# Kernel optimization log

Measured on AMD Instinct MI355X. Metric: run time of the kernel, lower is better.

## Reference

```python
import jax, jax.numpy as jnp
import numpy as np

COST_CLASS = 1.0
COST_BBOX = 5.0
COST_GIOU = 2.0
EPS = 1e-6

BS, Q, T = 8, 900, 256   # batch, num_queries, max_text_len
M = 2000                 # total target boxes concatenated over batch


def setup_inputs() -> dict:
    key = jax.random.key(0)
    k1, k2, k3, k4 = jax.random.split(key, 4)
    pred_logits = jax.random.normal(k1, (BS, Q, T), dtype=jnp.float32)
    pred_boxes = jax.random.uniform(k2, (BS, Q, 4), dtype=jnp.float32, minval=0.05, maxval=0.95)
    tgt_boxes = jax.random.uniform(k3, (M, 4), dtype=jnp.float32, minval=0.05, maxval=0.95)
    tgt_labels = jax.random.uniform(k4, (M, T), dtype=jnp.float32)  # positive token map (soft)
    return {"pred_logits": pred_logits, "pred_boxes": pred_boxes,
            "tgt_boxes": tgt_boxes, "tgt_labels": tgt_labels}


def box_cxcywh_to_xyxy(b):
    cx, cy, w, h = b[..., 0], b[..., 1], b[..., 2], b[..., 3]
    return jnp.stack([cx - 0.5 * w, cy - 0.5 * h, cx + 0.5 * w, cy + 0.5 * h], axis=-1)


def generalized_box_iou(boxes1, boxes2):
    # boxes1: [N,4] xyxy, boxes2: [M,4] xyxy -> [N,M] GIoU
    area1 = (boxes1[:, 2] - boxes1[:, 0]) * (boxes1[:, 3] - boxes1[:, 1])
    area2 = (boxes2[:, 2] - boxes2[:, 0]) * (boxes2[:, 3] - boxes2[:, 1])
    lt = jnp.maximum(boxes1[:, None, :2], boxes2[None, :, :2])  # [N,M,2]
    rb = jnp.minimum(boxes1[:, None, 2:], boxes2[None, :, 2:])
    wh = jnp.clip(rb - lt, 0.0)
    inter = wh[..., 0] * wh[..., 1]
    union = area1[:, None] + area2[None, :] - inter
    iou = inter / (union + EPS)
    lt_e = jnp.minimum(boxes1[:, None, :2], boxes2[None, :, :2])
    rb_e = jnp.maximum(boxes1[:, None, 2:], boxes2[None, :, 2:])
    wh_e = jnp.clip(rb_e - lt_e, 0.0)
    area_e = wh_e[..., 0] * wh_e[..., 1]
    return iou - (area_e - union) / (area_e + EPS)


def reference(pred_logits, pred_boxes, tgt_boxes, tgt_labels):
    bs, q, t = pred_logits.shape
    out_prob = jnp.clip(jax.nn.sigmoid(pred_logits.reshape(bs * q, t)), EPS, 1.0 - EPS)
    pred_bbox = pred_boxes.reshape(bs * q, 4)
    # normalized positive token map
    norm_labels = tgt_labels / (jnp.sum(tgt_labels, axis=1, keepdims=True) + EPS)
    # classification cost: -sum_t p[n,t] * map[m,t]  -> [N, M]
    cost_class = -jnp.einsum('nt,mt->nm', out_prob, norm_labels)
    # L1 box cost (cdist p=1) on cxcywh
    cost_bbox = jnp.sum(jnp.abs(pred_bbox[:, None, :] - tgt_boxes[None, :, :]), axis=-1)
    # GIoU cost on xyxy, clamped to >= -1
    giou = generalized_box_iou(box_cxcywh_to_xyxy(pred_bbox), box_cxcywh_to_xyxy(tgt_boxes))
    cost_giou = -jnp.clip(giou, -1.0)
    C = COST_BBOX * cost_bbox + COST_CLASS * cost_class + COST_GIOU * cost_giou
    return C.reshape(bs, q, -1)
```

## Files before the change

kernel.cpp:

```cpp
#include <hip/hip_runtime.h>
#include <math.h>

#define EPSF 1e-6f

typedef __attribute__((ext_vector_type(8))) short bf16x8;
typedef __attribute__((ext_vector_type(4))) float f32x4;
typedef __attribute__((ext_vector_type(4))) unsigned short u16x4;
typedef __attribute__((ext_vector_type(8))) unsigned short u16x8;

constexpr int TT = 256, MT = 2000, NP = 7200;

static __device__ __forceinline__ unsigned short f2bf(float f) {
    unsigned int u = __float_as_uint(f);
    u += 0x7FFFu + ((u >> 16) & 1u);
    return (unsigned short)(u >> 16);
}
static __device__ __forceinline__ float frcp(float x) { return __builtin_amdgcn_rcpf(x); }

static __device__ __forceinline__ void gload_lds16(const unsigned short* g, unsigned short* l) {
    __builtin_amdgcn_global_load_lds(
        (const __attribute__((address_space(1))) unsigned int*)(g),
        (__attribute__((address_space(3))) unsigned int*)(l),
        16, 0, 0);
}

__global__ __launch_bounds__(256) void prep_kernel(const float* __restrict__ logits,
                                                   const float* __restrict__ lab,
                                                   unsigned short* __restrict__ probs,
                                                   unsigned short* __restrict__ nlab) {
    int b = blockIdx.x;
    if (b < 900) {
        int i = (b * 256 + threadIdx.x) * 8;
        float4 x0 = *reinterpret_cast<const float4*>(logits + i);
        float4 x1 = *reinterpret_cast<const float4*>(logits + i + 4);
        float v[8] = {x0.x, x0.y, x0.z, x0.w, x1.x, x1.y, x1.z, x1.w};
        u16x8 o;
#pragma unroll
        for (int j = 0; j < 8; ++j) {
            float s = frcp(1.0f + __expf(-v[j]));
            s = fminf(fmaxf(s, EPSF), 1.0f - EPSF);
            o[j] = f2bf(s);
        }
        *reinterpret_cast<u16x8*>(probs + i) = o;
    } else {
        int wave = threadIdx.x >> 6;
        int lane = threadIdx.x & 63;
        int m = (b - 900) * 4 + wave;
        float4 v = reinterpret_cast<const float4*>(lab)[m * (TT / 4) + lane];
        float s = v.x + v.y + v.z + v.w;
#pragma unroll
        for (int off = 32; off > 0; off >>= 1) s += __shfl_down(s, off);
        float inv = frcp(__shfl(s, 0) + EPSF);
        u16x4 o;
        o[0] = f2bf(v.x * inv); o[1] = f2bf(v.y * inv);
        o[2] = f2bf(v.z * inv); o[3] = f2bf(v.w * inv);
        *reinterpret_cast<u16x4*>(nlab + m * TT + lane * 4) = o;
    }
}

constexpr int NTX = 113, NTY = 32;

__global__ __launch_bounds__(256) void cost_mfma_kernel(
    const unsigned short* __restrict__ A,
    const unsigned short* __restrict__ B,
    const float* __restrict__ pbox,
    const float* __restrict__ tbox,
    float* __restrict__ out)
{
    __shared__ __align__(16) unsigned short As[64 * 256];
    __shared__ __align__(16) unsigned short Bs[64 * 256];

    int n = blockIdx.x;
    int l = (n & 7) * 452 + (n >> 3);
    const int n0 = (l >> 5) * 64;
    const int m0 = (l & 31) * 64;

    const int tid = threadIdx.x;
    const int lane = tid & 63, wave = tid >> 6;
    const int wr = wave & 1, wc = wave >> 1;
    const int fr = lane & 15, quad = lane >> 4;

    float4 tb[2]; int mj[2]; bool mv[2];
#pragma unroll
    for (int tj = 0; tj < 2; ++tj) {
        int gm = m0 + wc * 32 + tj * 16 + fr;
        mv[tj] = gm < MT; mj[tj] = gm;
        int g = mv[tj] ? gm : MT - 1;
        tb[tj] = *reinterpret_cast<const float4*>(&tbox[g * 4]);
    }
    float4 pbv[2][4]; int pr[2][4];
#pragma unroll
    for (int ti = 0; ti < 2; ++ti)
#pragma unroll
        for (int r = 0; r < 4; ++r) {
            int p = n0 + wr * 32 + ti * 16 + quad * 4 + r;
            pr[ti][r] = p;
            int g = p < NP ? p : NP - 1;
            pbv[ti][r] = *reinterpret_cast<const float4*>(&pbox[g * 4]);
        }

    {
        const int lro = lane >> 5;
        const int lch = lane & 31;
#pragma unroll
        for (int i = 0; i < 8; ++i) {
            int row = wave * 16 + i * 2 + lro;
            int cs = (lch * 16) ^ ((row & 7) << 4);
            int gn = n0 + row; gn = gn > NP - 1 ? NP - 1 : gn;
            int gm = m0 + row; gm = gm > MT - 1 ? MT - 1 : gm;
            gload_lds16(A + gn * TT + (cs >> 1), &As[wave * 4096 + i * 512]);
            gload_lds16(B + gm * TT + (cs >> 1), &Bs[wave * 4096 + i * 512]);
        }
    }
    __syncthreads();

    const char* aB[2]; const char* bB[2];
    const int xs = (fr & 7) << 4;
#pragma unroll
    for (int t = 0; t < 2; ++t) {
        aB[t] = reinterpret_cast<const char*>(As) + (wr * 32 + t * 16 + fr) * 512;
        bB[t] = reinterpret_cast<const char*>(Bs) + (wc * 32 + t * 16 + fr) * 512;
    }

    f32x4 acc[2][2] = {};
#pragma unroll
    for (int kk = 0; kk < 8; ++kk) {
        int cb = (kk * 64 + quad * 16) ^ xs;
        bf16x8 af[2], bg[2];
#pragma unroll
        for (int t = 0; t < 2; ++t) {
            af[t] = *reinterpret_cast<const bf16x8*>(aB[t] + cb);
            bg[t] = *reinterpret_cast<const bf16x8*>(bB[t] + cb);
        }
#pragma unroll
        for (int ti = 0; ti < 2; ++ti)
#pragma unroll
            for (int tj = 0; tj < 2; ++tj)
                acc[ti][tj] = __builtin_amdgcn_mfma_f32_16x16x32_bf16(
                    af[ti], bg[tj], acc[ti][tj], 0, 0, 0);
    }

    float bcx[2], bcy[2], bww[2], bhh[2], bx1[2], by1[2], bx2[2], by2[2], areaB[2];
#pragma unroll
    for (int tj = 0; tj < 2; ++tj) {
        float4 b = tb[tj];
        bcx[tj] = b.x; bcy[tj] = b.y; bww[tj] = b.z; bhh[tj] = b.w;
        bx1[tj] = b.x - 0.5f * b.z; by1[tj] = b.y - 0.5f * b.w;
        bx2[tj] = b.x + 0.5f * b.z; by2[tj] = b.y + 0.5f * b.w;
        areaB[tj] = (bx2[tj] - bx1[tj]) * (by2[tj] - by1[tj]);
    }

#pragma unroll
    for (int ti = 0; ti < 2; ++ti) {
#pragma unroll
        for (int r = 0; r < 4; ++r) {
            int p = pr[ti][r];
            if (p >= NP) continue;
            float4 pb4 = pbv[ti][r];
            float ax1 = pb4.x - 0.5f * pb4.z, ay1 = pb4.y - 0.5f * pb4.w;
            float ax2 = pb4.x + 0.5f * pb4.z, ay2 = pb4.y + 0.5f * pb4.w;
            float areaA = (ax2 - ax1) * (ay2 - ay1);
#pragma unroll
            for (int tj = 0; tj < 2; ++tj) {
                if (!mv[tj]) continue;
                float l1 = fabsf(pb4.x - bcx[tj]) + fabsf(pb4.y - bcy[tj]) +
                           fabsf(pb4.z - bww[tj]) + fabsf(pb4.w - bhh[tj]);
                float ltx = fmaxf(ax1, bx1[tj]), lty = fmaxf(ay1, by1[tj]);
                float rbx = fminf(ax2, bx2[tj]), rby = fminf(ay2, by2[tj]);
                float iw = fmaxf(rbx - ltx, 0.0f), ih = fmaxf(rby - lty, 0.0f);
                float inter = iw * ih;
                float uni = areaA + areaB[tj] - inter;
                float iou = inter * frcp(uni + EPSF);
                float ex1 = fminf(ax1, bx1[tj]), ey1 = fminf(ay1, by1[tj]);
                float ex2 = fmaxf(ax2, bx2[tj]), ey2 = fmaxf(ay2, by2[tj]);
                float ew = fmaxf(ex2 - ex1, 0.0f), eh = fmaxf(ey2 - ey1, 0.0f);
                float areaE = ew * eh;
                float giou = iou - (areaE - uni) * frcp(areaE + EPSF);
                float res = 5.0f * l1 - acc[ti][tj][r] - 2.0f * fmaxf(giou, -1.0f);
                out[p * MT + mj[tj]] = res;
            }
        }
    }
}

extern "C" void kernel_launch(void* const* d_in, const int* in_sizes, int n_in,
                              void* d_out, int out_size, void* d_ws, size_t ws_size,
                              hipStream_t stream) {
    const float* pred_logits = (const float*)d_in[0];
    const float* pred_boxes  = (const float*)d_in[1];
    const float* tgt_boxes   = (const float*)d_in[2];
    const float* tgt_labels  = (const float*)d_in[3];
    float* out = (float*)d_out;

    unsigned short* probs = (unsigned short*)d_ws;
    unsigned short* nlab  = probs + NP * TT;

    prep_kernel<<<900 + 500, 256, 0, stream>>>(pred_logits, tgt_labels, probs, nlab);

    cost_mfma_kernel<<<NTX * NTY, 256, 0, stream>>>(probs, nlab, pred_boxes, tgt_boxes, out);
}
```

Baseline: 111.0 us.

## Load B fragments straight to registers, drop B LDS tile, raise occupancy

Removes the shared-memory staging of the normalized-label (B) tile. Each wave now loads its B MFMA fragments directly from global memory into registers, so LDS use per block is halved. The box loads are moved to after the matmul to lower register pressure, and launch bounds request 4 blocks per SM for higher occupancy. In exchange, B rows are re-read from global/L2 by both row-waves rather than shared through LDS, the direct loads use uncoalesced 16-byte strided accesses, and 16 bf16x8 registers are held per thread.

```diff
diff --git a/kernel.cpp b/kernel.cpp
--- a/kernel.cpp
+++ b/kernel.cpp
@@ -60,7 +60,7 @@
 
 constexpr int NTX = 113, NTY = 32;
 
-__global__ __launch_bounds__(256) void cost_mfma_kernel(
+__global__ __launch_bounds__(256, 4) void cost_mfma_kernel(
     const unsigned short* __restrict__ A,
     const unsigned short* __restrict__ B,
     const float* __restrict__ pbox,
@@ -68,7 +68,6 @@
     float* __restrict__ out)
 {
     __shared__ __align__(16) unsigned short As[64 * 256];
-    __shared__ __align__(16) unsigned short Bs[64 * 256];
 
     int n = blockIdx.x;
     int l = (n & 7) * 452 + (n >> 3);
@@ -80,24 +79,18 @@
     const int wr = wave & 1, wc = wave >> 1;
     const int fr = lane & 15, quad = lane >> 4;
 
-    float4 tb[2]; int mj[2]; bool mv[2];
+    const unsigned short* bp[2];
 #pragma unroll
-    for (int tj = 0; tj < 2; ++tj) {
-        int gm = m0 + wc * 32 + tj * 16 + fr;
-        mv[tj] = gm < MT; mj[tj] = gm;
-        int g = mv[tj] ? gm : MT - 1;
-        tb[tj] = *reinterpret_cast<const float4*>(&tbox[g * 4]);
+    for (int t = 0; t < 2; ++t) {
+        int gb = m0 + wc * 32 + t * 16 + fr; if (gb > MT - 1) gb = MT - 1;
+        bp[t] = B + gb * TT + quad * 8;
     }
-    float4 pbv[2][4]; int pr[2][4];
+    bf16x8 bg[2][8];
 #pragma unroll
-    for (int ti = 0; ti < 2; ++ti)
+    for (int kk = 0; kk < 8; ++kk)
 #pragma unroll
-        for (int r = 0; r < 4; ++r) {
-            int p = n0 + wr * 32 + ti * 16 + quad * 4 + r;
-            pr[ti][r] = p;
-            int g = p < NP ? p : NP - 1;
-            pbv[ti][r] = *reinterpret_cast<const float4*>(&pbox[g * 4]);
-        }
+        for (int t = 0; t < 2; ++t)
+            bg[t][kk] = *reinterpret_cast<const bf16x8*>(bp[t] + kk * 32);
 
     {
         const int lro = lane >> 5;
@@ -107,43 +100,41 @@
             int row = wave * 16 + i * 2 + lro;
             int cs = (lch * 16) ^ ((row & 7) << 4);
             int gn = n0 + row; gn = gn > NP - 1 ? NP - 1 : gn;
-            int gm = m0 + row; gm = gm > MT - 1 ? MT - 1 : gm;
             gload_lds16(A + gn * TT + (cs >> 1), &As[wave * 4096 + i * 512]);
-            gload_lds16(B + gm * TT + (cs >> 1), &Bs[wave * 4096 + i * 512]);
         }
     }
     __syncthreads();
 
-    const char* aB[2]; const char* bB[2];
+    const char* aB[2];
     const int xs = (fr & 7) << 4;
 #pragma unroll
-    for (int t = 0; t < 2; ++t) {
+    for (int t = 0; t < 2; ++t)
         aB[t] = reinterpret_cast<const char*>(As) + (wr * 32 + t * 16 + fr) * 512;
-        bB[t] = reinterpret_cast<const char*>(Bs) + (wc * 32 + t * 16 + fr) * 512;
-    }
 
     f32x4 acc[2][2] = {};
 #pragma unroll
     for (int kk = 0; kk < 8; ++kk) {
         int cb = (kk * 64 + quad * 16) ^ xs;
-        bf16x8 af[2], bg[2];
+        bf16x8 af[2];
 #pragma unroll
-        for (int t = 0; t < 2; ++t) {
+        for (int t = 0; t < 2; ++t)
             af[t] = *reinterpret_cast<const bf16x8*>(aB[t] + cb);
-            bg[t] = *reinterpret_cast<const bf16x8*>(bB[t] + cb);
-        }
 #pragma unroll
         for (int ti = 0; ti < 2; ++ti)
 #pragma unroll
             for (int tj = 0; tj < 2; ++tj)
                 acc[ti][tj] = __builtin_amdgcn_mfma_f32_16x16x32_bf16(
-                    af[ti], bg[tj], acc[ti][tj], 0, 0, 0);
+                    af[ti], bg[tj][kk], acc[ti][tj], 0, 0, 0);
     }
 
     float bcx[2], bcy[2], bww[2], bhh[2], bx1[2], by1[2], bx2[2], by2[2], areaB[2];
+    int mj[2]; bool mv[2];
 #pragma unroll
     for (int tj = 0; tj < 2; ++tj) {
-        float4 b = tb[tj];
+        int gm = m0 + wc * 32 + tj * 16 + fr;
+        mv[tj] = gm < MT; mj[tj] = gm;
+        int g = mv[tj] ? gm : MT - 1;
+        float4 b = *reinterpret_cast<const float4*>(&tbox[g * 4]);
         bcx[tj] = b.x; bcy[tj] = b.y; bww[tj] = b.z; bhh[tj] = b.w;
         bx1[tj] = b.x - 0.5f * b.z; by1[tj] = b.y - 0.5f * b.w;
         bx2[tj] = b.x + 0.5f * b.z; by2[tj] = b.y + 0.5f * b.w;
@@ -154,9 +145,9 @@
     for (int ti = 0; ti < 2; ++ti) {
 #pragma unroll
         for (int r = 0; r < 4; ++r) {
-            int p = pr[ti][r];
+            int p = n0 + wr * 32 + ti * 16 + quad * 4 + r;
             if (p >= NP) continue;
-            float4 pb4 = pbv[ti][r];
+            float4 pb4 = *reinterpret_cast<const float4*>(&pbox[p * 4]);
             float ax1 = pb4.x - 0.5f * pb4.z, ay1 = pb4.y - 0.5f * pb4.w;
             float ax2 = pb4.x + 0.5f * pb4.z, ay2 = pb4.y + 0.5f * pb4.w;
             float areaA = (ax2 - ax1) * (ay2 - ay1);
```

After: 124.4 us. 12.0% more time.

## Make cost kernel persistent and prefetch next tile during epilogue

Applied to the files above, without the earlier changes.

Replaces the one-tile-per-block grid (3616 blocks) with 512 persistent blocks that loop over tiles within an XCD slab, stride 64. After the MFMA phase, the block issues the async global-to-LDS loads and box loads for the next tile before running the GIoU/L1 epilogue and output stores for the current one. This overlaps load latency with the store-heavy epilogue and cuts block launch overhead. In exchange it adds extra syncs per tile and register pressure from the prefetched box data, and it sets launch bounds for two blocks per CU and raises MFMA priority with setprio.

```diff
diff --git a/kernel.cpp b/kernel.cpp
--- a/kernel.cpp
+++ b/kernel.cpp
@@ -59,8 +59,14 @@
 }
 
 constexpr int NTX = 113, NTY = 32;
-
-__global__ __launch_bounds__(256) void cost_mfma_kernel(
+constexpr int SLAB = 452;
+
+struct BoxPre {
+    float4 tb0, tb1;
+    float4 pb[8];
+};
+
+__global__ __launch_bounds__(256, 2) void cost_mfma_kernel(
     const unsigned short* __restrict__ A,
     const unsigned short* __restrict__ B,
     const float* __restrict__ pbox,
@@ -70,116 +76,148 @@
     __shared__ __align__(16) unsigned short As[64 * 256];
     __shared__ __align__(16) unsigned short Bs[64 * 256];
 
-    int n = blockIdx.x;
-    int l = (n & 7) * 452 + (n >> 3);
-    const int n0 = (l >> 5) * 64;
-    const int m0 = (l & 31) * 64;
+    const int x = blockIdx.x & 7;
+    const int kb = blockIdx.x >> 3;
 
     const int tid = threadIdx.x;
     const int lane = tid & 63, wave = tid >> 6;
     const int wr = wave & 1, wc = wave >> 1;
     const int fr = lane & 15, quad = lane >> 4;
 
-    float4 tb[2]; int mj[2]; bool mv[2];
-#pragma unroll
-    for (int tj = 0; tj < 2; ++tj) {
-        int gm = m0 + wc * 32 + tj * 16 + fr;
-        mv[tj] = gm < MT; mj[tj] = gm;
-        int g = mv[tj] ? gm : MT - 1;
-        tb[tj] = *reinterpret_cast<const float4*>(&tbox[g * 4]);
-    }
-    float4 pbv[2][4]; int pr[2][4];
-#pragma unroll
-    for (int ti = 0; ti < 2; ++ti)
-#pragma unroll
-        for (int r = 0; r < 4; ++r) {
-            int p = n0 + wr * 32 + ti * 16 + quad * 4 + r;
-            pr[ti][r] = p;
-            int g = p < NP ? p : NP - 1;
-            pbv[ti][r] = *reinterpret_cast<const float4*>(&pbox[g * 4]);
-        }
-
-    {
-        const int lro = lane >> 5;
-        const int lch = lane & 31;
-#pragma unroll
-        for (int i = 0; i < 8; ++i) {
-            int row = wave * 16 + i * 2 + lro;
-            int cs = (lch * 16) ^ ((row & 7) << 4);
-            int gn = n0 + row; gn = gn > NP - 1 ? NP - 1 : gn;
-            int gm = m0 + row; gm = gm > MT - 1 ? MT - 1 : gm;
-            gload_lds16(A + gn * TT + (cs >> 1), &As[wave * 4096 + i * 512]);
-            gload_lds16(B + gm * TT + (cs >> 1), &Bs[wave * 4096 + i * 512]);
-        }
-    }
-    __syncthreads();
-
+    const int lro = lane >> 5;
+    const int lch = lane & 31;
+
+    const int xs = (fr & 7) << 4;
     const char* aB[2]; const char* bB[2];
-    const int xs = (fr & 7) << 4;
 #pragma unroll
     for (int t = 0; t < 2; ++t) {
         aB[t] = reinterpret_cast<const char*>(As) + (wr * 32 + t * 16 + fr) * 512;
         bB[t] = reinterpret_cast<const char*>(Bs) + (wc * 32 + t * 16 + fr) * 512;
     }
 
-    f32x4 acc[2][2] = {};
-#pragma unroll
-    for (int kk = 0; kk < 8; ++kk) {
-        int cb = (kk * 64 + quad * 16) ^ xs;
-        bf16x8 af[2], bg[2];
-#pragma unroll
-        for (int t = 0; t < 2; ++t) {
-            af[t] = *reinterpret_cast<const bf16x8*>(aB[t] + cb);
-            bg[t] = *reinterpret_cast<const bf16x8*>(bB[t] + cb);
+    auto stage = [&](int n0_, int m0_) {
+#pragma unroll
+        for (int i = 0; i < 8; ++i) {
+            int row = wave * 16 + i * 2 + lro;
+            int cs = (lch * 16) ^ ((row & 7) << 4);
+            int gn = n0_ + row; gn = gn > NP - 1 ? NP - 1 : gn;
+            gload_lds16(A + gn * TT + (cs >> 1), &As[wave * 4096 + i * 512]);
+        }
+#pragma unroll
+        for (int i = 0; i < 8; ++i) {
+            int row = wave * 16 + i * 2 + lro;
+            int cs = (lch * 16) ^ ((row & 7) << 4);
+            int gm = m0_ + row; gm = gm > MT - 1 ? MT - 1 : gm;
+            gload_lds16(B + gm * TT + (cs >> 1), &Bs[wave * 4096 + i * 512]);
+        }
+    };
+    auto boxload = [&](int n0_, int m0_, BoxPre& bx) {
+        {
+            int gm = m0_ + wc * 32 + fr;
+            int g = gm < MT ? gm : MT - 1;
+            bx.tb0 = *reinterpret_cast<const float4*>(&tbox[g * 4]);
+        }
+        {
+            int gm = m0_ + wc * 32 + 16 + fr;
+            int g = gm < MT ? gm : MT - 1;
+            bx.tb1 = *reinterpret_cast<const float4*>(&tbox[g * 4]);
         }
 #pragma unroll
         for (int ti = 0; ti < 2; ++ti)
 #pragma unroll
-            for (int tj = 0; tj < 2; ++tj)
-                acc[ti][tj] = __builtin_amdgcn_mfma_f32_16x16x32_bf16(
-                    af[ti], bg[tj], acc[ti][tj], 0, 0, 0);
-    }
-
-    float bcx[2], bcy[2], bww[2], bhh[2], bx1[2], by1[2], bx2[2], by2[2], areaB[2];
-#pragma unroll
-    for (int tj = 0; tj < 2; ++tj) {
-        float4 b = tb[tj];
-        bcx[tj] = b.x; bcy[tj] = b.y; bww[tj] = b.z; bhh[tj] = b.w;
-        bx1[tj] = b.x - 0.5f * b.z; by1[tj] = b.y - 0.5f * b.w;
-        bx2[tj] = b.x + 0.5f * b.z; by2[tj] = b.y + 0.5f * b.w;
-        areaB[tj] = (bx2[tj] - bx1[tj]) * (by2[tj] - by1[tj]);
-    }
-
-#pragma unroll
-    for (int ti = 0; ti < 2; ++ti) {
-#pragma unroll
-        for (int r = 0; r < 4; ++r) {
-            int p = pr[ti][r];
-            if (p >= NP) continue;
-            float4 pb4 = pbv[ti][r];
-            float ax1 = pb4.x - 0.5f * pb4.z, ay1 = pb4.y - 0.5f * pb4.w;
-            float ax2 = pb4.x + 0.5f * pb4.z, ay2 = pb4.y + 0.5f * pb4.w;
-            float areaA = (ax2 - ax1) * (ay2 - ay1);
-#pragma unroll
-            for (int tj = 0; tj < 2; ++tj) {
-                if (!mv[tj]) continue;
-                float l1 = fabsf(pb4.x - bcx[tj]) + fabsf(pb4.y - bcy[tj]) +
-                           fabsf(pb4.z - bww[tj]) + fabsf(pb4.w - bhh[tj]);
-                float ltx = fmaxf(ax1, bx1[tj]), lty = fmaxf(ay1, by1[tj]);
-                float rbx = fminf(ax2, bx2[tj]), rby = fminf(ay2, by2[tj]);
-                float iw = fmaxf(rbx - ltx, 0.0f), ih = fmaxf(rby - lty, 0.0f);
-                float inter = iw * ih;
-                float uni = areaA + areaB[tj] - inter;
-                float iou = inter * frcp(uni + EPSF);
-                float ex1 = fminf(ax1, bx1[tj]), ey1 = fminf(ay1, by1[tj]);
-                float ex2 = fmaxf(ax2, bx2[tj]), ey2 = fmaxf(ay2, by2[tj]);
-                float ew = fmaxf(ex2 - ex1, 0.0f), eh = fmaxf(ey2 - ey1, 0.0f);
-                float areaE = ew * eh;
-                float giou = iou - (areaE - uni) * frcp(areaE + EPSF);
-                float res = 5.0f * l1 - acc[ti][tj][r] - 2.0f * fmaxf(giou, -1.0f);
-                out[p * MT + mj[tj]] = res;
+            for (int r = 0; r < 4; ++r) {
+                int p = n0_ + wr * 32 + ti * 16 + quad * 4 + r;
+                int g = p < NP ? p : NP - 1;
+                bx.pb[ti * 4 + r] = *reinterpret_cast<const float4*>(&pbox[g * 4]);
             }
-        }
+    };
+
+    int joff = kb;
+    int l = x * SLAB + joff;
+    int n0 = (l >> 5) * 64, m0 = (l & 31) * 64;
+    stage(n0, m0);
+    BoxPre nxt; boxload(n0, m0, nxt);
+
+    for (;;) {
+        __syncthreads();
+        BoxPre cur = nxt;
+        const int cn0 = n0, cm0 = m0;
+
+        f32x4 acc[2][2] = {};
+        __builtin_amdgcn_s_setprio(1);
+#pragma unroll
+        for (int kk = 0; kk < 8; ++kk) {
+            int cb = (kk * 64 + quad * 16) ^ xs;
+            bf16x8 af[2], bg[2];
+#pragma unroll
+            for (int t = 0; t < 2; ++t) {
+                af[t] = *reinterpret_cast<const bf16x8*>(aB[t] + cb);
+                bg[t] = *reinterpret_cast<const bf16x8*>(bB[t] + cb);
+            }
+#pragma unroll
+            for (int ti = 0; ti < 2; ++ti)
+#pragma unroll
+                for (int tj = 0; tj < 2; ++tj)
+                    acc[ti][tj] = __builtin_amdgcn_mfma_f32_16x16x32_bf16(
+                        af[ti], bg[tj], acc[ti][tj], 0, 0, 0);
+        }
+        __builtin_amdgcn_s_setprio(0);
+        __syncthreads();
+
+        const bool more = (joff + 64) < SLAB;
+        if (more) {
+            joff += 64;
+            l = x * SLAB + joff;
+            n0 = (l >> 5) * 64; m0 = (l & 31) * 64;
+            stage(n0, m0);
+            boxload(n0, m0, nxt);
+        }
+
+        float bcx[2], bcy[2], bww[2], bhh[2], bx1[2], by1[2], bx2[2], by2[2], areaB[2];
+        int mj[2]; bool mv[2];
+#pragma unroll
+        for (int tj = 0; tj < 2; ++tj) {
+            int gm = cm0 + wc * 32 + tj * 16 + fr;
+            mv[tj] = gm < MT; mj[tj] = gm;
+            float4 b = tj ? cur.tb1 : cur.tb0;
+            bcx[tj] = b.x; bcy[tj] = b.y; bww[tj] = b.z; bhh[tj] = b.w;
+            bx1[tj] = b.x - 0.5f * b.z; by1[tj] = b.y - 0.5f * b.w;
+            bx2[tj] = b.x + 0.5f * b.z; by2[tj] = b.y + 0.5f * b.w;
+            areaB[tj] = (bx2[tj] - bx1[tj]) * (by2[tj] - by1[tj]);
+        }
+
+#pragma unroll
+        for (int ti = 0; ti < 2; ++ti) {
+#pragma unroll
+            for (int r = 0; r < 4; ++r) {
+                int p = cn0 + wr * 32 + ti * 16 + quad * 4 + r;
+                if (p >= NP) continue;
+                float4 pb4 = cur.pb[ti * 4 + r];
+                float ax1 = pb4.x - 0.5f * pb4.z, ay1 = pb4.y - 0.5f * pb4.w;
+                float ax2 = pb4.x + 0.5f * pb4.z, ay2 = pb4.y + 0.5f * pb4.w;
+                float areaA = (ax2 - ax1) * (ay2 - ay1);
+#pragma unroll
+                for (int tj = 0; tj < 2; ++tj) {
+                    if (!mv[tj]) continue;
+                    float l1 = fabsf(pb4.x - bcx[tj]) + fabsf(pb4.y - bcy[tj]) +
+                               fabsf(pb4.z - bww[tj]) + fabsf(pb4.w - bhh[tj]);
+                    float ltx = fmaxf(ax1, bx1[tj]), lty = fmaxf(ay1, by1[tj]);
+                    float rbx = fminf(ax2, bx2[tj]), rby = fminf(ay2, by2[tj]);
+                    float iw = fmaxf(rbx - ltx, 0.0f), ih = fmaxf(rby - lty, 0.0f);
+                    float inter = iw * ih;
+                    float uni = areaA + areaB[tj] - inter;
+                    float iou = inter * frcp(uni + EPSF);
+                    float ex1 = fminf(ax1, bx1[tj]), ey1 = fminf(ay1, by1[tj]);
+                    float ex2 = fmaxf(ax2, bx2[tj]), ey2 = fmaxf(ay2, by2[tj]);
+                    float ew = fmaxf(ex2 - ex1, 0.0f), eh = fmaxf(ey2 - ey1, 0.0f);
+                    float areaE = ew * eh;
+                    float giou = iou - (areaE - uni) * frcp(areaE + EPSF);
+                    float res = 5.0f * l1 - acc[ti][tj][r] - 2.0f * fmaxf(giou, -1.0f);
+                    out[p * MT + mj[tj]] = res;
+                }
+            }
+        }
+        if (!more) break;
     }
 }
 
@@ -197,5 +235,5 @@
 
     prep_kernel<<<900 + 500, 256, 0, stream>>>(pred_logits, tgt_labels, probs, nlab);
 
-    cost_mfma_kernel<<<NTX * NTY, 256, 0, stream>>>(probs, nlab, pred_boxes, tgt_boxes, out);
-}
+    cost_mfma_kernel<<<512, 256, 0, stream>>>(probs, nlab, pred_boxes, tgt_boxes, out);
+}
```

Result: no change. 113.1 us (+1.8%).
